# Kernel optimization log

Measured on AMD Instinct MI355X. Metric: run time of the kernel, lower is better.

The kernel has to match this reference:

```python
import jax, jax.numpy as jnp
import numpy as np

N, E = 100000, 600000
IN, H = 164, 128
NH = 4  # attention heads over embed_dim H//4 = 32


def layer_norm(x, g, b, eps=1e-5):
    m = x.mean(-1, keepdims=True)
    v = x.var(-1, keepdims=True)
    return (x - m) * jax.lax.rsqrt(v + eps) * g + b


def gcn_conv(x, W, b, src, dst, n):
    # PyG GCNConv: add self-loops, symmetric D^{-1/2}(A+I)D^{-1/2} normalization.
    deg = jnp.ones((n,), x.dtype).at[dst].add(1.0)  # degree of A+I on target nodes
    dinv = jax.lax.rsqrt(deg)
    xw = x @ W  # [n, out]
    msg = xw[src] * (dinv[src] * dinv[dst])[:, None]  # gather + edge-norm
    agg = jax.ops.segment_sum(msg, dst, num_segments=n)  # scatter-add
    agg = agg + xw * (dinv * dinv)[:, None]  # self-loop term
    return agg + b


def mha_seq1(x, Wq, bq, Wk, bk, Wv, bv, Wo, bo):
    # nn.MultiheadAttention with seq_len==1: softmax over a single key -> weights==1.
    dh = x.shape[-1] // NH
    q = (x @ Wq + bq).reshape(-1, NH, dh)
    k = (x @ Wk + bk).reshape(-1, NH, dh)
    v = (x @ Wv + bv).reshape(-1, NH, dh)
    scores = jnp.sum(q * k, -1, keepdims=True) / jnp.sqrt(jnp.float32(dh))  # [n,NH,1]
    attn = jax.nn.softmax(scores[..., None], axis=-1)[..., 0]  # all ones, kept for fidelity
    out = (attn * v).reshape(-1, NH * dh)
    return out @ Wo + bo


def setup_inputs() -> dict:
    key = jax.random.key(0)
    ks = jax.random.split(key, 16)

    def kaiming(k, i, o):
        return jax.random.normal(k, (i, o), jnp.float32) * (2.0 / i) ** 0.5

    Ha, Hb, Hc = H, H // 2, H // 4  # 128, 64, 32
    return {
        "x": jax.random.normal(ks[0], (N, IN), jnp.float32),
        "edge_index": jax.random.randint(ks[1], (2, E), 0, N),
        "Wi": kaiming(ks[2], IN, Ha), "bi": jnp.zeros((Ha,), jnp.float32),
        "g1": jnp.ones((Ha,), jnp.float32), "b1": jnp.zeros((Ha,), jnp.float32),
        "Wg1": kaiming(ks[3], Ha, Ha), "bg1": jnp.zeros((Ha,), jnp.float32),
        "Wg2": kaiming(ks[4], Ha, Hb), "bg2": jnp.zeros((Hb,), jnp.float32),
        "g2": jnp.ones((Hb,), jnp.float32), "b2": jnp.zeros((Hb,), jnp.float32),
        "Wg3": kaiming(ks[5], Hb, Hc), "bg3": jnp.zeros((Hc,), jnp.float32),
        "Wq": kaiming(ks[6], Hc, Hc), "bq": jnp.zeros((Hc,), jnp.float32),
        "Wk": kaiming(ks[7], Hc, Hc), "bk": jnp.zeros((Hc,), jnp.float32),
        "Wv": kaiming(ks[8], Hc, Hc), "bv": jnp.zeros((Hc,), jnp.float32),
        "Wo": kaiming(ks[9], Hc, Hc), "bo": jnp.zeros((Hc,), jnp.float32),
        "Wc1": kaiming(ks[10], Hc, H // 8), "bc1": jnp.zeros((H // 8,), jnp.float32),
        "Wc2": kaiming(ks[11], H // 8, 32), "bc2": jnp.zeros((32,), jnp.float32),
        "Wc3": kaiming(ks[12], 32, 1), "bc3": jnp.zeros((1,), jnp.float32),
    }


def reference(x, edge_index, Wi, bi, g1, b1, Wg1, bg1, Wg2, bg2, g2, b2,
              Wg3, bg3, Wq, bq, Wk, bk, Wv, bv, Wo, bo,
              Wc1, bc1, Wc2, bc2, Wc3, bc3):
    src, dst = edge_index[0], edge_index[1]
    n = x.shape[0]
    # dropout layers are identity in eval mode
    h = layer_norm(jax.nn.relu(x @ Wi + bi), g1, b1)
    h1 = jax.nn.relu(gcn_conv(h, Wg1, bg1, src, dst, n)) + h
    h2 = layer_norm(jax.nn.relu(gcn_conv(h1, Wg2, bg2, src, dst, n)), g2, b2)
    h3 = jax.nn.relu(gcn_conv(h2, Wg3, bg3, src, dst, n))
    h3 = mha_seq1(h3, Wq, bq, Wk, bk, Wv, bv, Wo, bo)
    h3 = jax.nn.relu(h3 @ Wc1 + bc1)
    h3 = jax.nn.relu(h3 @ Wc2 + bc2)
    return (h3 @ Wc3 + bc3)[:, 0]
```

## Files before the change

kernel.cpp:

```cpp
#include <hip/hip_runtime.h>


typedef __attribute__((ext_vector_type(8))) _Float16 f16x8;
typedef __attribute__((ext_vector_type(4))) _Float16 f16x4;
typedef __attribute__((ext_vector_type(4))) float f32x4;

__global__ void k_zero_int(int* __restrict__ p, int n) {
  int i = blockIdx.x * blockDim.x + threadIdx.x;
  if (i < n) p[i] = 0;
}

__global__ void k_count(const int* __restrict__ dst, int* __restrict__ counts, int e) {
  int i = blockIdx.x * blockDim.x + threadIdx.x;
  if (i < e) atomicAdd(&counts[dst[i]], 1);
}

__global__ __launch_bounds__(256) void k_scan_part(
    const int* __restrict__ counts, int* __restrict__ bsums, int n) {
  int tid = threadIdx.x;
  int i0 = blockIdx.x * 1024 + tid * 4;
  int s = 0;
#pragma unroll
  for (int k = 0; k < 4; k++) { int i = i0 + k; if (i < n) s += counts[i]; }
#pragma unroll
  for (int d = 1; d < 64; d <<= 1) s += __shfl_xor(s, d);
  __shared__ int wsum[4];
  int lane = tid & 63, w = tid >> 6;
  if (lane == 0) wsum[w] = s;
  __syncthreads();
  if (tid == 0) bsums[blockIdx.x] = wsum[0] + wsum[1] + wsum[2] + wsum[3];
}

__global__ __launch_bounds__(128) void k_scan_top(int* __restrict__ bsums, int nb) {
  int tid = threadIdx.x;
  int orig = (tid < nb) ? bsums[tid] : 0;
  int v = orig;
  int lane = tid & 63, w = tid >> 6;
#pragma unroll
  for (int d = 1; d < 64; d <<= 1) { int t = __shfl_up(v, d); if (lane >= d) v += t; }
  __shared__ int ws[2];
  if (lane == 63) ws[w] = v;
  __syncthreads();
  if (w == 1) v += ws[0];
  if (tid < nb) bsums[tid] = v - orig;
}

__global__ __launch_bounds__(256) void k_scan_down(
    const int* __restrict__ counts, const int* __restrict__ bsums,
    int* __restrict__ offsets, float* __restrict__ dinv, int n, int e) {
  int tid = threadIdx.x;
  int i0 = blockIdx.x * 1024 + tid * 4;
  int c[4]; int tsum = 0;
#pragma unroll
  for (int k = 0; k < 4; k++) { int i = i0 + k; c[k] = (i < n) ? counts[i] : 0; tsum += c[k]; }
  int v = tsum;
  int lane = tid & 63, w = tid >> 6;
#pragma unroll
  for (int d = 1; d < 64; d <<= 1) { int t = __shfl_up(v, d); if (lane >= d) v += t; }
  __shared__ int wsum[4];
  if (lane == 63) wsum[w] = v;
  __syncthreads();
  int wadd = 0;
#pragma unroll
  for (int q = 0; q < 4; q++) if (q < w) wadd += wsum[q];
  int run = (v - tsum) + wadd + bsums[blockIdx.x];
#pragma unroll
  for (int k = 0; k < 4; k++) {
    int i = i0 + k;
    if (i < n) { offsets[i] = run; dinv[i] = rsqrtf((float)(c[k] + 1)); }
    run += c[k];
  }
  if (blockIdx.x == 0 && tid == 0) offsets[n] = e;
}

__global__ void k_fill(const int* __restrict__ src, const int* __restrict__ dst,
                       const int* __restrict__ offsets, int* __restrict__ cursor,
                       const float* __restrict__ dinv, int2* __restrict__ csr, int e) {
  int i = blockIdx.x * blockDim.x + threadIdx.x;
  if (i >= e) return;
  int s = src[i], d = dst[i];
  int pos = atomicAdd(&cursor[d], 1);
  csr[offsets[d] + pos] = make_int2(s, __float_as_int(dinv[s] * dinv[d]));
}

__device__ __forceinline__ void pack_hi(const float* __restrict__ W,
                                        _Float16* __restrict__ dst,
                                        int K, int N, int u) {
  int lane = u & 63; int rest = u >> 6; int CT = N >> 4;
  int ct = rest % CT, ks = rest / CT;
  int gcol = ct * 16 + (lane & 15);
  int gk0 = ks * 32 + (lane >> 4) * 8;
  size_t o = (size_t)(ks * CT + ct) * 512 + lane * 8;
#pragma unroll
  for (int i = 0; i < 8; i++) {
    float v = (gk0 + i < K) ? W[(size_t)(gk0 + i) * N + gcol] : 0.0f;
    dst[o + i] = (_Float16)v;
  }
}

__device__ __forceinline__ void pack_hl(const float* __restrict__ W,
                                        _Float16* __restrict__ dst,
                                        int K, int N, int u) {
  int lane = u & 63; int rest = u >> 6; int CT = N >> 4;
  int ct = rest % CT, ks = rest / CT;
  int gcol = ct * 16 + (lane & 15);
  int gk0 = ks * 32 + (lane >> 4) * 8;
  size_t oh = (size_t)((ks * CT + ct) * 2) * 512 + lane * 8;
#pragma unroll
  for (int i = 0; i < 8; i++) {
    float v = (gk0 + i < K) ? W[(size_t)(gk0 + i) * N + gcol] : 0.0f;
    _Float16 h = (_Float16)v;
    dst[oh + i] = h;
    dst[oh + 512 + i] = (_Float16)(v - (float)h);
  }
}

__global__ void k_prepack(const float* __restrict__ Wi, const float* __restrict__ Wg1,
                          const float* __restrict__ Wg2, const float* __restrict__ Wg3,
                          _Float16* __restrict__ pWi, _Float16* __restrict__ pWg1,
                          _Float16* __restrict__ pWg2, _Float16* __restrict__ pWg3) {
  int t = blockIdx.x * blockDim.x + threadIdx.x;
  if (t < 3072) pack_hi(Wi, pWi, 164, 128, t);
  else if (t < 5120) pack_hl(Wg1, pWg1, 128, 128, t - 3072);
  else if (t < 6144) pack_hl(Wg2, pWg2, 128, 64, t - 5120);
  else if (t < 6400) pack_hl(Wg3, pWg3, 64, 32, t - 6144);
}

__global__ __launch_bounds__(512) void k_gemm_in(
    const float* __restrict__ x, const _Float16* __restrict__ pB,
    const float* __restrict__ bias, const float* __restrict__ gamma,
    const float* __restrict__ beta, _Float16* __restrict__ out, int n) {
  constexpr int K = 164, N = 128, KS = 6, CT = 8;
  __shared__ __align__(16) _Float16 sB[KS * CT * 512];
  int tid = threadIdx.x;
  {
    const f16x8* s = (const f16x8*)pB;
    f16x8* d = (f16x8*)sB;
    for (int i = tid; i < KS * CT * 64; i += 512) d[i] = s[i];
  }
  __syncthreads();
  int lane = tid & 63, w = tid >> 6;
  int row = blockIdx.x * 128 + w * 16 + (lane & 15);
  bool rv = row < n;
  const float* ar = x + (size_t)row * K;
  int kof = (lane >> 4) * 8;
  f32x4 acc[CT];
#pragma unroll
  for (int c = 0; c < CT; c++) acc[c] = (f32x4)0.0f;
  for (int ks = 0; ks < KS; ks++) {
    int gk = ks * 32 + kof;
    float v[8];
    if (rv && gk + 8 <= K) {
      const float4* p = (const float4*)(ar + gk);
      float4 u0 = p[0], u1 = p[1];
      v[0] = u0.x; v[1] = u0.y; v[2] = u0.z; v[3] = u0.w;
      v[4] = u1.x; v[5] = u1.y; v[6] = u1.z; v[7] = u1.w;
    } else {
#pragma unroll
      for (int i = 0; i < 8; i++) v[i] = (rv && gk + i < K) ? ar[gk + i] : 0.0f;
    }
    f16x8 ah, al;
#pragma unroll
    for (int i = 0; i < 8; i++) {
      ah[i] = (_Float16)v[i];
      al[i] = (_Float16)(v[i] - (float)ah[i]);
    }
#pragma unroll
    for (int c = 0; c < CT; c++) {
      f16x8 b = ((const f16x8*)sB)[(ks * CT + c) * 64 + lane];
      acc[c] = __builtin_amdgcn_mfma_f32_16x16x32_f16(ah, b, acc[c], 0, 0, 0);
      acc[c] = __builtin_amdgcn_mfma_f32_16x16x32_f16(al, b, acc[c], 0, 0, 0);
    }
  }
  int r0 = (lane >> 4) * 4;
  int li = lane & 15;
  float s1[4] = {0, 0, 0, 0}, s2[4] = {0, 0, 0, 0};
#pragma unroll
  for (int c = 0; c < CT; c++) {
    float bb = bias[c * 16 + li];
#pragma unroll
    for (int r = 0; r < 4; r++) {
      float t = acc[c][r] + bb;
      t = t > 0.0f ? t : 0.0f;
      acc[c][r] = t;
      s1[r] += t;
      s2[r] += t * t;
    }
  }
#pragma unroll
  for (int m = 1; m < 16; m <<= 1) {
#pragma unroll
    for (int r = 0; r < 4; r++) {
      s1[r] += __shfl_xor(s1[r], m);
      s2[r] += __shfl_xor(s2[r], m);
    }
  }
#pragma unroll
  for (int c = 0; c < CT; c++) {
    float gv = gamma[c * 16 + li], bv = beta[c * 16 + li];
#pragma unroll
    for (int r = 0; r < 4; r++) {
      int node = blockIdx.x * 128 + w * 16 + r0 + r;
      if (node < n) {
        float mean = s1[r] * (1.0f / N);
        float var = s2[r] * (1.0f / N) - mean * mean;
        float rs = rsqrtf(var + 1e-5f);
        out[(size_t)node * N + c * 16 + li] =
            (_Float16)((acc[c][r] - mean) * rs * gv + bv);
      }
    }
  }
}

template <int K, int N>
__global__ __launch_bounds__(512) void k_gemm_f16(
    const _Float16* __restrict__ A, const _Float16* __restrict__ pB,
    _Float16* __restrict__ out, int n) {
  constexpr int KS = K / 32, CT = N / 16;
  __shared__ __align__(16) _Float16 sB[KS * CT * 1024];
  int tid = threadIdx.x;
  {
    const f16x8* s = (const f16x8*)pB;
    f16x8* d = (f16x8*)sB;
    for (int i = tid; i < KS * CT * 128; i += 512) d[i] = s[i];
  }
  __syncthreads();
  int lane = tid & 63, w = tid >> 6;
  int row = blockIdx.x * 128 + w * 16 + (lane & 15);
  bool rv = row < n;
  const _Float16* ar = A + (size_t)row * K + (lane >> 4) * 8;
  f32x4 acc[CT];
#pragma unroll
  for (int c = 0; c < CT; c++) acc[c] = (f32x4)0.0f;
  for (int ks = 0; ks < KS; ks++) {
    f16x8 av;
    if (rv) av = *(const f16x8*)(ar + ks * 32);
    else {
#pragma unroll
      for (int i = 0; i < 8; i++) av[i] = (_Float16)0.0f;
    }
#pragma unroll
    for (int c = 0; c < CT; c++) {
      f16x8 bh = ((const f16x8*)sB)[((ks * CT + c) * 2) * 64 + lane];
      f16x8 bl = ((const f16x8*)sB)[((ks * CT + c) * 2 + 1) * 64 + lane];
      acc[c] = __builtin_amdgcn_mfma_f32_16x16x32_f16(av, bh, acc[c], 0, 0, 0);
      acc[c] = __builtin_amdgcn_mfma_f32_16x16x32_f16(av, bl, acc[c], 0, 0, 0);
    }
  }
  int r0 = (lane >> 4) * 4;
  int li = lane & 15;
#pragma unroll
  for (int c = 0; c < CT; c++) {
#pragma unroll
    for (int r = 0; r < 4; r++) {
      int node = blockIdx.x * 128 + w * 16 + r0 + r;
      if (node < n) out[(size_t)node * N + c * 16 + li] = (_Float16)acc[c][r];
    }
  }
}

template <int OUT_D, int MODE>
__global__ __launch_bounds__(256) void k_gather(
    const int* __restrict__ off, const int2* __restrict__ csr,
    const _Float16* __restrict__ xw, const float* __restrict__ dinv,
    const float* __restrict__ bias, const _Float16* __restrict__ auxh,
    const float* __restrict__ gamma, const float* __restrict__ beta,
    _Float16* __restrict__ out, int n) {
  constexpr int TPN = OUT_D / 4;
  constexpr int NPB = 256 / TPN;
  int tid = threadIdx.x;
  int node = blockIdx.x * NPB + tid / TPN;
  int li = tid % TPN;
  if (node >= n) return;
  int start = off[node], end = off[node + 1];
  float di = dinv[node];
  float d2 = di * di;
  const _Float16* xp = xw + 4 * li;
  f16x4 self = *(const f16x4*)(xp + (size_t)node * OUT_D);
  float a0 = (float)self[0] * d2 + bias[4 * li + 0];
  float a1 = (float)self[1] * d2 + bias[4 * li + 1];
  float a2 = (float)self[2] * d2 + bias[4 * li + 2];
  float a3 = (float)self[3] * d2 + bias[4 * li + 3];
  for (int base = start; base < end; base += TPN) {
    int m = end - base; if (m > TPN) m = TPN;
    int sv = 0; float nv = 0.0f;
    if (li < m) { int2 me = csr[base + li]; sv = me.x; nv = __int_as_float(me.y); }
    int j = 0;
    for (; j + 4 <= m; j += 4) {
      int s0 = __shfl(sv, j + 0, TPN); float w0 = __shfl(nv, j + 0, TPN);
      int s1 = __shfl(sv, j + 1, TPN); float w1 = __shfl(nv, j + 1, TPN);
      int s2 = __shfl(sv, j + 2, TPN); float w2 = __shfl(nv, j + 2, TPN);
      int s3 = __shfl(sv, j + 3, TPN); float w3 = __shfl(nv, j + 3, TPN);
      f16x4 v0 = *(const f16x4*)(xp + (size_t)s0 * OUT_D);
      f16x4 v1 = *(const f16x4*)(xp + (size_t)s1 * OUT_D);
      f16x4 v2 = *(const f16x4*)(xp + (size_t)s2 * OUT_D);
      f16x4 v3 = *(const f16x4*)(xp + (size_t)s3 * OUT_D);
      a0 += (float)v0[0] * w0 + (float)v1[0] * w1 + (float)v2[0] * w2 + (float)v3[0] * w3;
      a1 += (float)v0[1] * w0 + (float)v1[1] * w1 + (float)v2[1] * w2 + (float)v3[1] * w3;
      a2 += (float)v0[2] * w0 + (float)v1[2] * w1 + (float)v2[2] * w2 + (float)v3[2] * w3;
      a3 += (float)v0[3] * w0 + (float)v1[3] * w1 + (float)v2[3] * w2 + (float)v3[3] * w3;
    }
    for (; j < m; j++) {
      int s = __shfl(sv, j, TPN); float wj = __shfl(nv, j, TPN);
      f16x4 v = *(const f16x4*)(xp + (size_t)s * OUT_D);
      a0 += (float)v[0] * wj; a1 += (float)v[1] * wj;
      a2 += (float)v[2] * wj; a3 += (float)v[3] * wj;
    }
  }
  _Float16* po = out + (size_t)node * OUT_D + 4 * li;
  if constexpr (MODE == 0) {
    f16x4 hres = *(const f16x4*)(auxh + (size_t)node * OUT_D + 4 * li);
    f16x4 o;
    o[0] = (_Float16)((a0 > 0.0f ? a0 : 0.0f) + (float)hres[0]);
    o[1] = (_Float16)((a1 > 0.0f ? a1 : 0.0f) + (float)hres[1]);
    o[2] = (_Float16)((a2 > 0.0f ? a2 : 0.0f) + (float)hres[2]);
    o[3] = (_Float16)((a3 > 0.0f ? a3 : 0.0f) + (float)hres[3]);
    *(f16x4*)po = o;
  } else if constexpr (MODE == 1) {
    float v0 = a0 > 0.0f ? a0 : 0.0f, v1 = a1 > 0.0f ? a1 : 0.0f;
    float v2 = a2 > 0.0f ? a2 : 0.0f, v3 = a3 > 0.0f ? a3 : 0.0f;
    float s1 = v0 + v1 + v2 + v3;
    float s2 = v0 * v0 + v1 * v1 + v2 * v2 + v3 * v3;
#pragma unroll
    for (int d = 1; d < TPN; d <<= 1) {
      s1 += __shfl_xor(s1, d, TPN);
      s2 += __shfl_xor(s2, d, TPN);
    }
    float m_ = s1 * (1.0f / OUT_D);
    float var = s2 * (1.0f / OUT_D) - m_ * m_;
    float rs = rsqrtf(var + 1e-5f);
    f16x4 o;
    o[0] = (_Float16)((v0 - m_) * rs * gamma[4 * li + 0] + beta[4 * li + 0]);
    o[1] = (_Float16)((v1 - m_) * rs * gamma[4 * li + 1] + beta[4 * li + 1]);
    o[2] = (_Float16)((v2 - m_) * rs * gamma[4 * li + 2] + beta[4 * li + 2]);
    o[3] = (_Float16)((v3 - m_) * rs * gamma[4 * li + 3] + beta[4 * li + 3]);
    *(f16x4*)po = o;
  } else {
    f16x4 o;
    o[0] = (_Float16)a0; o[1] = (_Float16)a1;
    o[2] = (_Float16)a2; o[3] = (_Float16)a3;
    *(f16x4*)po = o;
  }
}

__global__ __launch_bounds__(256) void k_tail(
    const _Float16* __restrict__ agg3, const float* __restrict__ Wv,
    const float* __restrict__ bv, const float* __restrict__ Wo,
    const float* __restrict__ bo, const float* __restrict__ Wc1,
    const float* __restrict__ bc1, const float* __restrict__ Wc2,
    const float* __restrict__ bc2, const float* __restrict__ Wc3,
    const float* __restrict__ bc3, float* __restrict__ out, int n) {
  __shared__ float sWv[1024], sWo[1024], sWc1[512], sWc2[512];
  __shared__ float sbv[32], sbo[32], sbc2[32], sWc3[32], sbc1[16], sbc3[1];
  int tid = threadIdx.x;
  for (int i = tid; i < 1024; i += 256) { sWv[i] = Wv[i]; sWo[i] = Wo[i]; }
  for (int i = tid; i < 512; i += 256) { sWc1[i] = Wc1[i]; sWc2[i] = Wc2[i]; }
  if (tid < 32) { sbv[tid] = bv[tid]; sbo[tid] = bo[tid];
                  sbc2[tid] = bc2[tid]; sWc3[tid] = Wc3[tid]; }
  if (tid < 16) sbc1[tid] = bc1[tid];
  if (tid == 0) sbc3[0] = bc3[0];
  __syncthreads();
  int node = blockIdx.x * blockDim.x + tid;
  if (node >= n) return;
  float a[32];
  const f16x8* row8 = (const f16x8*)(agg3 + (size_t)node * 32);
#pragma unroll
  for (int q = 0; q < 4; q++) {
    f16x8 t = row8[q];
#pragma unroll
    for (int i = 0; i < 8; i++) {
      float f = (float)t[i];
      a[8 * q + i] = f > 0.0f ? f : 0.0f;
    }
  }
  float v[32];
#pragma unroll
  for (int j = 0; j < 32; j++) v[j] = sbv[j];
  for (int k = 0; k < 32; k++) {
#pragma unroll
    for (int j = 0; j < 32; j++) v[j] += a[k] * sWv[k * 32 + j];
  }
  float o[32];
#pragma unroll
  for (int j = 0; j < 32; j++) o[j] = sbo[j];
  for (int k = 0; k < 32; k++) {
#pragma unroll
    for (int j = 0; j < 32; j++) o[j] += v[k] * sWo[k * 32 + j];
  }
  float c1[16];
#pragma unroll
  for (int j = 0; j < 16; j++) c1[j] = sbc1[j];
  for (int k = 0; k < 32; k++) {
#pragma unroll
    for (int j = 0; j < 16; j++) c1[j] += o[k] * sWc1[k * 16 + j];
  }
#pragma unroll
  for (int j = 0; j < 16; j++) c1[j] = c1[j] > 0.0f ? c1[j] : 0.0f;
  float c2[32];
#pragma unroll
  for (int j = 0; j < 32; j++) c2[j] = sbc2[j];
  for (int k = 0; k < 16; k++) {
#pragma unroll
    for (int j = 0; j < 32; j++) c2[j] += c1[k] * sWc2[k * 32 + j];
  }
  float r = sbc3[0];
#pragma unroll
  for (int k = 0; k < 32; k++) {
    float c = c2[k] > 0.0f ? c2[k] : 0.0f;
    r += c * sWc3[k];
  }
  out[node] = r;
}

extern "C" void kernel_launch(void* const* d_in, const int* in_sizes, int n_in,
                              void* d_out, int out_size, void* d_ws, size_t ws_size,
                              hipStream_t stream) {
  const float* x   = (const float*)d_in[0];
  const int* ei    = (const int*)d_in[1];
  const float* Wi  = (const float*)d_in[2];
  const float* bi  = (const float*)d_in[3];
  const float* g1  = (const float*)d_in[4];
  const float* b1  = (const float*)d_in[5];
  const float* Wg1 = (const float*)d_in[6];
  const float* bg1 = (const float*)d_in[7];
  const float* Wg2 = (const float*)d_in[8];
  const float* bg2 = (const float*)d_in[9];
  const float* g2  = (const float*)d_in[10];
  const float* b2  = (const float*)d_in[11];
  const float* Wg3 = (const float*)d_in[12];
  const float* bg3 = (const float*)d_in[13];
  const float* Wv  = (const float*)d_in[18];
  const float* bv  = (const float*)d_in[19];
  const float* Wo  = (const float*)d_in[20];
  const float* bo  = (const float*)d_in[21];
  const float* Wc1 = (const float*)d_in[22];
  const float* bc1 = (const float*)d_in[23];
  const float* Wc2 = (const float*)d_in[24];
  const float* bc2 = (const float*)d_in[25];
  const float* Wc3 = (const float*)d_in[26];
  const float* bc3 = (const float*)d_in[27];

  const int n = in_sizes[0] / 164;
  const int e = in_sizes[1] / 2;
  const int* src = ei;
  const int* dst = ei + e;

  char* ws = (char*)d_ws;
  size_t off = 0;
  auto alloc = [&](size_t bytes) {
    char* p = ws + off;
    off += (bytes + 255) & ~(size_t)255;
    return p;
  };
  _Float16* A     = (_Float16*)alloc((size_t)n * 128 * 2);
  _Float16* B     = (_Float16*)alloc((size_t)n * 128 * 2);
  _Float16* C     = (_Float16*)alloc((size_t)n * 128 * 2);
  float* dinv     = (float*)alloc((size_t)n * 4);
  int*   counts   = (int*)alloc((size_t)n * 4);
  int*   offsets  = (int*)alloc((size_t)(n + 1) * 4);
  int*   bsums    = (int*)alloc(128 * 4);
  int2*  csr      = (int2*)alloc((size_t)e * 8);
  _Float16* pWi   = (_Float16*)alloc(6 * 8 * 512 * 2);
  _Float16* pWg1  = (_Float16*)alloc(4 * 8 * 1024 * 2);
  _Float16* pWg2  = (_Float16*)alloc(4 * 4 * 1024 * 2);
  _Float16* pWg3  = (_Float16*)alloc(2 * 2 * 1024 * 2);
  (void)ws_size;

  const int BS = 256;
  const int SB = (n + 1023) / 1024;
  const int GB = (n + 127) / 128;

  k_prepack<<<25, 256, 0, stream>>>(Wi, Wg1, Wg2, Wg3, pWi, pWg1, pWg2, pWg3);

  k_zero_int<<<(n + BS - 1) / BS, BS, 0, stream>>>(counts, n);
  k_count<<<(e + BS - 1) / BS, BS, 0, stream>>>(dst, counts, e);
  k_scan_part<<<SB, 256, 0, stream>>>(counts, bsums, n);
  k_scan_top<<<1, 128, 0, stream>>>(bsums, SB);
  k_scan_down<<<SB, 256, 0, stream>>>(counts, bsums, offsets, dinv, n, e);
  k_zero_int<<<(n + BS - 1) / BS, BS, 0, stream>>>(counts, n);
  k_fill<<<(e + BS - 1) / BS, BS, 0, stream>>>(src, dst, offsets, counts, dinv,
                                               csr, e);

  k_gemm_in<<<GB, 512, 0, stream>>>(x, pWi, bi, g1, b1, A, n);

  k_gemm_f16<128, 128><<<GB, 512, 0, stream>>>(A, pWg1, B, n);
  k_gather<128, 0><<<(n + 7) / 8, 256, 0, stream>>>(
      offsets, csr, B, dinv, bg1, A, nullptr, nullptr, C, n);

  k_gemm_f16<128, 64><<<GB, 512, 0, stream>>>(C, pWg2, A, n);
  k_gather<64, 1><<<(n + 15) / 16, 256, 0, stream>>>(
      offsets, csr, A, dinv, bg2, nullptr, g2, b2, B, n);

  k_gemm_f16<64, 32><<<GB, 512, 0, stream>>>(B, pWg3, A, n);
  k_gather<32, 2><<<(n + 31) / 32, 256, 0, stream>>>(
      offsets, csr, A, dinv, bg3, nullptr, nullptr, nullptr, C, n);

  k_tail<<<(n + BS - 1) / BS, BS, 0, stream>>>(
      C, Wv, bv, Wo, bo, Wc1, bc1, Wc2, bc2, Wc3, bc3, (float*)d_out, n);
}
```

Baseline: 234.9 us.

## Fuse zeroing into setup/scan kernels and batch loads in GEMMs and gathers

```diff
diff --git a/kernel.cpp b/kernel.cpp
--- a/kernel.cpp
+++ b/kernel.cpp
@@ -4,11 +4,6 @@
 typedef __attribute__((ext_vector_type(8))) _Float16 f16x8;
 typedef __attribute__((ext_vector_type(4))) _Float16 f16x4;
 typedef __attribute__((ext_vector_type(4))) float f32x4;
-
-__global__ void k_zero_int(int* __restrict__ p, int n) {
-  int i = blockIdx.x * blockDim.x + threadIdx.x;
-  if (i < n) p[i] = 0;
-}
 
 __global__ void k_count(const int* __restrict__ dst, int* __restrict__ counts, int e) {
   int i = blockIdx.x * blockDim.x + threadIdx.x;
@@ -46,7 +41,7 @@
 }
 
 __global__ __launch_bounds__(256) void k_scan_down(
-    const int* __restrict__ counts, const int* __restrict__ bsums,
+    int* __restrict__ counts, const int* __restrict__ bsums,
     int* __restrict__ offsets, float* __restrict__ dinv, int n, int e) {
   int tid = threadIdx.x;
   int i0 = blockIdx.x * 1024 + tid * 4;
@@ -67,7 +62,11 @@
 #pragma unroll
   for (int k = 0; k < 4; k++) {
     int i = i0 + k;
-    if (i < n) { offsets[i] = run; dinv[i] = rsqrtf((float)(c[k] + 1)); }
+    if (i < n) {
+      offsets[i] = run;
+      dinv[i] = rsqrtf((float)(c[k] + 1));
+      counts[i] = 0;
+    }
     run += c[k];
   }
   if (blockIdx.x == 0 && tid == 0) offsets[n] = e;
@@ -115,49 +114,64 @@
   }
 }
 
-__global__ void k_prepack(const float* __restrict__ Wi, const float* __restrict__ Wg1,
-                          const float* __restrict__ Wg2, const float* __restrict__ Wg3,
-                          _Float16* __restrict__ pWi, _Float16* __restrict__ pWg1,
-                          _Float16* __restrict__ pWg2, _Float16* __restrict__ pWg3) {
-  int t = blockIdx.x * blockDim.x + threadIdx.x;
-  if (t < 3072) pack_hi(Wi, pWi, 164, 128, t);
-  else if (t < 5120) pack_hl(Wg1, pWg1, 128, 128, t - 3072);
-  else if (t < 6144) pack_hl(Wg2, pWg2, 128, 64, t - 5120);
-  else if (t < 6400) pack_hl(Wg3, pWg3, 64, 32, t - 6144);
+__global__ void k_setup(const float* __restrict__ Wi, const float* __restrict__ Wg1,
+                        const float* __restrict__ Wg2, const float* __restrict__ Wg3,
+                        _Float16* __restrict__ pWi, _Float16* __restrict__ pWg1,
+                        _Float16* __restrict__ pWg2, _Float16* __restrict__ pWg3,
+                        int* __restrict__ counts, int n) {
+  int b = blockIdx.x;
+  if (b < 25) {
+    int t = b * 256 + threadIdx.x;
+    if (t < 3072) pack_hi(Wi, pWi, 164, 128, t);
+    else if (t < 5120) pack_hl(Wg1, pWg1, 128, 128, t - 3072);
+    else if (t < 6144) pack_hl(Wg2, pWg2, 128, 64, t - 5120);
+    else if (t < 6400) pack_hl(Wg3, pWg3, 64, 32, t - 6144);
+  } else {
+    int i = (b - 25) * 256 + threadIdx.x;
+    if (i < n) counts[i] = 0;
+  }
 }
 
 __global__ __launch_bounds__(512) void k_gemm_in(
     const float* __restrict__ x, const _Float16* __restrict__ pB,
     const float* __restrict__ bias, const float* __restrict__ gamma,
     const float* __restrict__ beta, _Float16* __restrict__ out, int n) {
-  constexpr int K = 164, N = 128, KS = 6, CT = 8;
-  __shared__ __align__(16) _Float16 sB[KS * CT * 512];
+  constexpr int K = 164, N = 128, CT = 8;
+  __shared__ __align__(16) _Float16 sB[6 * CT * 512];
   int tid = threadIdx.x;
   {
     const f16x8* s = (const f16x8*)pB;
     f16x8* d = (f16x8*)sB;
-    for (int i = tid; i < KS * CT * 64; i += 512) d[i] = s[i];
+    for (int i = tid; i < 6 * CT * 64; i += 512) d[i] = s[i];
   }
   __syncthreads();
   int lane = tid & 63, w = tid >> 6;
   int row = blockIdx.x * 128 + w * 16 + (lane & 15);
   bool rv = row < n;
-  const float* ar = x + (size_t)row * K;
   int kof = (lane >> 4) * 8;
+  float4 xv[11];
+#pragma unroll
+  for (int i = 0; i < 11; i++) xv[i] = make_float4(0.f, 0.f, 0.f, 0.f);
+  if (rv) {
+    const float4* p = (const float4*)(x + (size_t)row * K + kof);
+#pragma unroll
+    for (int ks = 0; ks < 5; ks++) { xv[2 * ks] = p[ks * 8]; xv[2 * ks + 1] = p[ks * 8 + 1]; }
+    if (kof == 0) xv[10] = *(const float4*)(x + (size_t)row * K + 160);
+  }
   f32x4 acc[CT];
 #pragma unroll
   for (int c = 0; c < CT; c++) acc[c] = (f32x4)0.0f;
-  for (int ks = 0; ks < KS; ks++) {
-    int gk = ks * 32 + kof;
+#pragma unroll
+  for (int ks = 0; ks < 6; ks++) {
     float v[8];
-    if (rv && gk + 8 <= K) {
-      const float4* p = (const float4*)(ar + gk);
-      float4 u0 = p[0], u1 = p[1];
+    if (ks < 5) {
+      float4 u0 = xv[2 * ks], u1 = xv[2 * ks + 1];
       v[0] = u0.x; v[1] = u0.y; v[2] = u0.z; v[3] = u0.w;
       v[4] = u1.x; v[5] = u1.y; v[6] = u1.z; v[7] = u1.w;
     } else {
-#pragma unroll
-      for (int i = 0; i < 8; i++) v[i] = (rv && gk + i < K) ? ar[gk + i] : 0.0f;
+      float4 u0 = xv[10];
+      v[0] = u0.x; v[1] = u0.y; v[2] = u0.z; v[3] = u0.w;
+      v[4] = 0.f; v[5] = 0.f; v[6] = 0.f; v[7] = 0.f;
     }
     f16x8 ah, al;
 #pragma unroll
@@ -229,22 +243,26 @@
   int row = blockIdx.x * 128 + w * 16 + (lane & 15);
   bool rv = row < n;
   const _Float16* ar = A + (size_t)row * K + (lane >> 4) * 8;
+  f16x8 av[KS];
+#pragma unroll
+  for (int ks = 0; ks < KS; ks++) {
+    if (rv) av[ks] = *(const f16x8*)(ar + ks * 32);
+    else {
+#pragma unroll
+      for (int i = 0; i < 8; i++) av[ks][i] = (_Float16)0.0f;
+    }
+  }
   f32x4 acc[CT];
 #pragma unroll
   for (int c = 0; c < CT; c++) acc[c] = (f32x4)0.0f;
+#pragma unroll
   for (int ks = 0; ks < KS; ks++) {
-    f16x8 av;
-    if (rv) av = *(const f16x8*)(ar + ks * 32);
-    else {
-#pragma unroll
-      for (int i = 0; i < 8; i++) av[i] = (_Float16)0.0f;
-    }
 #pragma unroll
     for (int c = 0; c < CT; c++) {
       f16x8 bh = ((const f16x8*)sB)[((ks * CT + c) * 2) * 64 + lane];
       f16x8 bl = ((const f16x8*)sB)[((ks * CT + c) * 2 + 1) * 64 + lane];
-      acc[c] = __builtin_amdgcn_mfma_f32_16x16x32_f16(av, bh, acc[c], 0, 0, 0);
-      acc[c] = __builtin_amdgcn_mfma_f32_16x16x32_f16(av, bl, acc[c], 0, 0, 0);
+      acc[c] = __builtin_amdgcn_mfma_f32_16x16x32_f16(av[ks], bh, acc[c], 0, 0, 0);
+      acc[c] = __builtin_amdgcn_mfma_f32_16x16x32_f16(av[ks], bl, acc[c], 0, 0, 0);
     }
   }
   int r0 = (lane >> 4) * 4;
@@ -281,30 +299,27 @@
   float a1 = (float)self[1] * d2 + bias[4 * li + 1];
   float a2 = (float)self[2] * d2 + bias[4 * li + 2];
   float a3 = (float)self[3] * d2 + bias[4 * li + 3];
-  for (int base = start; base < end; base += TPN) {
-    int m = end - base; if (m > TPN) m = TPN;
-    int sv = 0; float nv = 0.0f;
-    if (li < m) { int2 me = csr[base + li]; sv = me.x; nv = __int_as_float(me.y); }
-    int j = 0;
-    for (; j + 4 <= m; j += 4) {
-      int s0 = __shfl(sv, j + 0, TPN); float w0 = __shfl(nv, j + 0, TPN);
-      int s1 = __shfl(sv, j + 1, TPN); float w1 = __shfl(nv, j + 1, TPN);
-      int s2 = __shfl(sv, j + 2, TPN); float w2 = __shfl(nv, j + 2, TPN);
-      int s3 = __shfl(sv, j + 3, TPN); float w3 = __shfl(nv, j + 3, TPN);
-      f16x4 v0 = *(const f16x4*)(xp + (size_t)s0 * OUT_D);
-      f16x4 v1 = *(const f16x4*)(xp + (size_t)s1 * OUT_D);
-      f16x4 v2 = *(const f16x4*)(xp + (size_t)s2 * OUT_D);
-      f16x4 v3 = *(const f16x4*)(xp + (size_t)s3 * OUT_D);
-      a0 += (float)v0[0] * w0 + (float)v1[0] * w1 + (float)v2[0] * w2 + (float)v3[0] * w3;
-      a1 += (float)v0[1] * w0 + (float)v1[1] * w1 + (float)v2[1] * w2 + (float)v3[1] * w3;
-      a2 += (float)v0[2] * w0 + (float)v1[2] * w1 + (float)v2[2] * w2 + (float)v3[2] * w3;
-      a3 += (float)v0[3] * w0 + (float)v1[3] * w1 + (float)v2[3] * w2 + (float)v3[3] * w3;
-    }
-    for (; j < m; j++) {
-      int s = __shfl(sv, j, TPN); float wj = __shfl(nv, j, TPN);
-      f16x4 v = *(const f16x4*)(xp + (size_t)s * OUT_D);
-      a0 += (float)v[0] * wj; a1 += (float)v[1] * wj;
-      a2 += (float)v[2] * wj; a3 += (float)v[3] * wj;
+  for (int cb = start; cb < end; cb += TPN) {
+    int m = end - cb; if (m > TPN) m = TPN;
+    int sv = node; float nv = 0.0f;
+    if (li < m) { int2 me = csr[cb + li]; sv = me.x; nv = __int_as_float(me.y); }
+    for (int j0 = 0; j0 < m; j0 += 8) {
+      int s[8]; float wg[8];
+#pragma unroll
+      for (int q = 0; q < 8; q++) {
+        s[q] = __shfl(sv, j0 + q, TPN);
+        wg[q] = __shfl(nv, j0 + q, TPN);
+      }
+      f16x4 v[8];
+#pragma unroll
+      for (int q = 0; q < 8; q++) v[q] = *(const f16x4*)(xp + (size_t)s[q] * OUT_D);
+#pragma unroll
+      for (int q = 0; q < 8; q++) {
+        a0 += (float)v[q][0] * wg[q];
+        a1 += (float)v[q][1] * wg[q];
+        a2 += (float)v[q][2] * wg[q];
+        a3 += (float)v[q][3] * wg[q];
+      }
     }
   }
   _Float16* po = out + (size_t)node * OUT_D + 4 * li;
@@ -470,14 +485,13 @@
   const int SB = (n + 1023) / 1024;
   const int GB = (n + 127) / 128;
 
-  k_prepack<<<25, 256, 0, stream>>>(Wi, Wg1, Wg2, Wg3, pWi, pWg1, pWg2, pWg3);
-
-  k_zero_int<<<(n + BS - 1) / BS, BS, 0, stream>>>(counts, n);
+  k_setup<<<25 + (n + 255) / 256, 256, 0, stream>>>(
+      Wi, Wg1, Wg2, Wg3, pWi, pWg1, pWg2, pWg3, counts, n);
+
   k_count<<<(e + BS - 1) / BS, BS, 0, stream>>>(dst, counts, e);
   k_scan_part<<<SB, 256, 0, stream>>>(counts, bsums, n);
   k_scan_top<<<1, 128, 0, stream>>>(bsums, SB);
   k_scan_down<<<SB, 256, 0, stream>>>(counts, bsums, offsets, dinv, n, e);
-  k_zero_int<<<(n + BS - 1) / BS, BS, 0, stream>>>(counts, n);
   k_fill<<<(e + BS - 1) / BS, BS, 0, stream>>>(src, dst, offsets, counts, dinv,
                                                csr, e);
 
```

New measurement: 227.3 us. 3.2% less time.
